# Kernel tuning notes

Hardware: AMD Instinct MI355X
Metric: run time of the kernel (lower is better)

The kernel has to match this reference:

```python
import jax, jax.numpy as jnp
import numpy as np
import math

BSZ, SEQ, DM = 2, 2048, 2048
NH, NKV, HD = 16, 8, 128
INTER = 8192
THETA = 10000.0
EPS = 1e-6
SOFTCAP = 50.0


def quant_per_token(x):
    # dynamic per-token symmetric int8 quant: scale = max|x|/127
    s = jnp.max(jnp.abs(x), axis=-1, keepdims=True) / 127.0
    s = jnp.maximum(s, 1e-8)
    q = jnp.clip(jnp.round(x / s), -127.0, 127.0)
    return q, s


def quant_weight(w):
    # per-output-channel symmetric int8 quant (rows are out channels)
    s = jnp.max(jnp.abs(w), axis=1, keepdims=True) / 127.0
    q = jnp.clip(jnp.round(w / s), -127.0, 127.0)
    return q, s


def w8a8_linear(qx, sx, w):
    # int8 GEMM with fused dequant: (qx @ qw^T) * s_act * s_weight
    qw, sw = quant_weight(w)
    return (qx @ qw.T) * sx * sw.T


def rmsnorm_quant(x, w):
    # RMSNormGeneral: w * x / sqrt(mean(x^2)+eps), then per-token quant
    var = jnp.mean(x * x, axis=-1, keepdims=True)
    y = x * jax.lax.rsqrt(var + EPS) * w
    return quant_per_token(y)


def rope_tables(seqlen, dim, theta):
    inv_freq = 1.0 / theta ** (jnp.arange(0, dim, 2, dtype=jnp.float32) / dim)
    pos = jnp.arange(seqlen, dtype=jnp.float32)
    fh = pos[:, None] * inv_freq[None, :]            # [S, dim/2]
    freqs = jnp.concatenate([fh, fh], axis=-1)       # [S, dim]
    return jnp.cos(freqs), jnp.sin(freqs)


def apply_rope(x, cos, sin):
    # x: [B, S, H, D]; rotate-half RoPE
    d2 = x.shape[-1] // 2
    rot = jnp.concatenate([-x[..., d2:], x[..., :d2]], axis=-1)
    return x * cos[None, :, None, :] + rot * sin[None, :, None, :]


def attention(q, k, v, mask, softcap):
    # q: [B, NH, S, D]; k, v: [B, NKV, S, D]
    groups = q.shape[1] // k.shape[1]
    if groups > 1:
        k = jnp.repeat(k, groups, axis=1)
        v = jnp.repeat(v, groups, axis=1)
    scores = jnp.einsum('bhqd,bhkd->bhqk', q, k) / math.sqrt(q.shape[-1])
    if softcap:
        scores = jnp.tanh(scores / softcap) * softcap
    scores = scores + mask
    attn = jax.nn.softmax(scores, axis=-1)
    out = jnp.einsum('bhqk,bhkd->bhqd', attn, v)
    return out.transpose(0, 2, 1, 3).reshape(q.shape[0], q.shape[2], -1)


def setup_inputs() -> dict:
    key = jax.random.key(0)
    ks = jax.random.split(key, 7)
    return {
        'hidden_states': jax.random.normal(ks[0], (BSZ, SEQ, DM), jnp.float32),
        'w_in_norm': jax.random.normal(ks[1], (DM,), jnp.float32) * 0.1 + 1.0,
        'w_post_norm': jax.random.normal(ks[2], (DM,), jnp.float32) * 0.1 + 1.0,
        'wqkv': jax.random.normal(ks[3], (NH * HD + 2 * NKV * HD, DM), jnp.float32) * 0.02,
        'wo': jax.random.normal(ks[4], (DM, NH * HD), jnp.float32) * 0.02,
        'w_gate_up': jax.random.normal(ks[5], (2 * INTER, DM), jnp.float32) * 0.02,
        'w_down': jax.random.normal(ks[6], (DM, INTER), jnp.float32) * 0.02,
    }


def reference(hidden_states, w_in_norm, w_post_norm, wqkv, wo, w_gate_up, w_down):
    q_dim, kv_dim = NH * HD, NKV * HD
    T = BSZ * SEQ
    x = hidden_states.reshape(T, DM)

    # --- attention block ---
    residual = x
    qx, sx = rmsnorm_quant(x, w_in_norm)
    qkv = w8a8_linear(qx, sx, wqkv)                      # [T, q_dim+2*kv_dim]
    q, k, v = jnp.split(qkv, [q_dim, q_dim + kv_dim], axis=-1)
    q = q.reshape(BSZ, SEQ, NH, HD)
    k = k.reshape(BSZ, SEQ, NKV, HD)
    v = v.reshape(BSZ, SEQ, NKV, HD).transpose(0, 2, 1, 3)

    cos, sin = rope_tables(SEQ, HD, THETA)
    q = apply_rope(q, cos, sin).transpose(0, 2, 1, 3)    # [B, NH, S, D]
    k = apply_rope(k, cos, sin).transpose(0, 2, 1, 3)    # [B, NKV, S, D]

    causal = jnp.tril(jnp.ones((SEQ, SEQ), dtype=bool))
    mask = jnp.where(causal, 0.0, -1e9).astype(jnp.float32)[None, None]
    attn_out = attention(q, k, v, mask, SOFTCAP).reshape(T, q_dim)

    qa, sa = quant_per_token(attn_out)
    x = residual + w8a8_linear(qa, sa, wo)

    # --- MLP block ---
    residual = x
    qx, sx = rmsnorm_quant(x, w_post_norm)
    gateup = w8a8_linear(qx, sx, w_gate_up)              # [T, 2*INTER]
    gate, up = jnp.split(gateup, 2, axis=-1)
    act = jax.nn.gelu(gate, approximate=True) * up       # gelu_and_mul
    qm, sm = quant_per_token(act)
    x = residual + w8a8_linear(qm, sm, w_down)

    return x.reshape(BSZ, SEQ, DM)
```

## Files before the change

### kernel.cpp

```cpp
#include <hip/hip_runtime.h>
#include <cstdint>
#include <math.h>

#define T_TOKENS 4096
#define SEQ 2048
#define DM 2048
#define NH 16
#define NKV 8
#define HD 128
#define QDIM 2048
#define KVDIM 1024
#define QKVN 4096
#define INTER 8192
#define GUN 16384

typedef int v4i __attribute__((ext_vector_type(4)));
typedef float v4f __attribute__((ext_vector_type(4)));
typedef short s8v __attribute__((ext_vector_type(8)));
typedef short s4v __attribute__((ext_vector_type(4)));
typedef short s2v __attribute__((ext_vector_type(2)));

#define GL16(g, l)                                                                       \
  __builtin_amdgcn_global_load_lds((__attribute__((address_space(1))) const void*)(g),   \
                                   (__attribute__((address_space(3))) void*)(l), 16, 0, 0)

__device__ inline float wave_sum(float v) {
#pragma unroll
  for (int off = 32; off > 0; off >>= 1) v += __shfl_down(v, off);
  return v;
}
__device__ inline float wave_max(float v) {
#pragma unroll
  for (int off = 32; off > 0; off >>= 1) v = fmaxf(v, __shfl_down(v, off));
  return v;
}
__device__ inline float dot4(float4 a, float4 b) {
  return a.x * b.x + a.y * b.y + a.z * b.z + a.w * b.w;
}
__device__ inline int8_t quant1(float v, float s) {
  float q = rintf(v / s);
  q = fminf(fmaxf(q, -127.f), 127.f);
  return (int8_t)(int)q;
}
__device__ inline unsigned short f2bf_rne(float x) {
  unsigned u = __float_as_uint(x);
  return (unsigned short)((u + 0x7FFFu + ((u >> 16) & 1u)) >> 16);
}
__device__ inline float bf2f(unsigned short h) { return __uint_as_float(((unsigned)h) << 16); }

__global__ void rope_table_kernel(float* __restrict__ cosT, float* __restrict__ sinT) {
  int s = blockIdx.x, d = threadIdx.x;
  float inv = 1.0f / powf(10000.0f, (float)d * (1.0f / 64.0f));
  float f = (float)s * inv;
  cosT[s * 64 + d] = cosf(f);
  sinT[s * 64 + d] = sinf(f);
}

__global__ __launch_bounds__(256) void quant_w_kernel(const float* __restrict__ w,
                                                      int8_t* __restrict__ qw,
                                                      float* __restrict__ sw, int K) {
  __shared__ float red[4];
  int row = blockIdx.x, tid = threadIdx.x;
  const float* wr = w + (size_t)row * K;
  int nv = K >> 10;
  float4 v[8];
  float mx = 0.f;
#pragma unroll
  for (int i = 0; i < 8; i++) {
    if (i < nv) {
      v[i] = *(const float4*)(wr + (size_t)(tid + i * 256) * 4);
      mx = fmaxf(mx, fmaxf(fmaxf(fabsf(v[i].x), fabsf(v[i].y)),
                           fmaxf(fabsf(v[i].z), fabsf(v[i].w))));
    }
  }
  mx = wave_max(mx);
  if ((tid & 63) == 0) red[tid >> 6] = mx;
  __syncthreads();
  float m = fmaxf(fmaxf(red[0], red[1]), fmaxf(red[2], red[3]));
  float s = m * (1.0f / 127.0f);
  if (tid == 0) sw[row] = s;
  float sd = (s > 0.f) ? s : 1.f;
  int8_t* qr = qw + (size_t)row * K;
#pragma unroll
  for (int i = 0; i < 8; i++) {
    if (i < nv) {
      char4 o;
      o.x = quant1(v[i].x, sd);
      o.y = quant1(v[i].y, sd);
      o.z = quant1(v[i].z, sd);
      o.w = quant1(v[i].w, sd);
      *(char4*)(qr + (size_t)(tid + i * 256) * 4) = o;
    }
  }
}

__global__ __launch_bounds__(256) void quant_w_gu_kernel(const float* __restrict__ w,
                                                         int8_t* __restrict__ qw,
                                                         float* __restrict__ sw) {
  __shared__ float red[4];
  int row = blockIdx.x, tid = threadIdx.x;
  const int K = DM;
  int j = (row < INTER) ? row : row - INTER;
  int pr = (j >> 6) * 128 + ((j >> 4) & 3) * 32 + ((row < INTER) ? 0 : 16) + (j & 15);
  const float* wr = w + (size_t)row * K;
  float4 v[2];
  float mx = 0.f;
#pragma unroll
  for (int i = 0; i < 2; i++) {
    v[i] = *(const float4*)(wr + (size_t)(tid + i * 256) * 4);
    mx = fmaxf(mx, fmaxf(fmaxf(fabsf(v[i].x), fabsf(v[i].y)),
                         fmaxf(fabsf(v[i].z), fabsf(v[i].w))));
  }
  mx = wave_max(mx);
  if ((tid & 63) == 0) red[tid >> 6] = mx;
  __syncthreads();
  float m = fmaxf(fmaxf(red[0], red[1]), fmaxf(red[2], red[3]));
  float s = m * (1.0f / 127.0f);
  if (tid == 0) sw[pr] = s;
  float sd = (s > 0.f) ? s : 1.f;
  int8_t* qr = qw + (size_t)pr * K;
#pragma unroll
  for (int i = 0; i < 2; i++) {
    char4 o;
    o.x = quant1(v[i].x, sd);
    o.y = quant1(v[i].y, sd);
    o.z = quant1(v[i].z, sd);
    o.w = quant1(v[i].w, sd);
    *(char4*)(qr + (size_t)(tid + i * 256) * 4) = o;
  }
}

__global__ __launch_bounds__(256) void rmsnorm_quant_kernel(const float* __restrict__ x,
                                                            const float* __restrict__ w,
                                                            int8_t* __restrict__ q,
                                                            float* __restrict__ s) {
  __shared__ float red[8];
  int t = blockIdx.x, tid = threadIdx.x;
  const float* xr = x + (size_t)t * DM;
  float4 a = *(const float4*)(xr + tid * 8);
  float4 b = *(const float4*)(xr + tid * 8 + 4);
  float ss = dot4(a, a) + dot4(b, b);
  ss = wave_sum(ss);
  if ((tid & 63) == 0) red[tid >> 6] = ss;
  __syncthreads();
  float tot = red[0] + red[1] + red[2] + red[3];
  float rms = rsqrtf(tot * (1.0f / DM) + 1e-6f);
  float4 wa = *(const float4*)(w + tid * 8);
  float4 wb = *(const float4*)(w + tid * 8 + 4);
  float y[8] = {a.x * rms * wa.x, a.y * rms * wa.y, a.z * rms * wa.z, a.w * rms * wa.w,
                b.x * rms * wb.x, b.y * rms * wb.y, b.z * rms * wb.z, b.w * rms * wb.w};
  float mx = 0.f;
#pragma unroll
  for (int i = 0; i < 8; i++) mx = fmaxf(mx, fabsf(y[i]));
  mx = wave_max(mx);
  if ((tid & 63) == 0) red[4 + (tid >> 6)] = mx;
  __syncthreads();
  float m = fmaxf(fmaxf(red[4], red[5]), fmaxf(red[6], red[7]));
  float sc = fmaxf(m * (1.0f / 127.0f), 1e-8f);
  if (tid == 0) s[t] = sc;
  int8_t* qr = q + (size_t)t * DM + tid * 8;
  char4 o0, o1;
  o0.x = quant1(y[0], sc); o0.y = quant1(y[1], sc); o0.z = quant1(y[2], sc); o0.w = quant1(y[3], sc);
  o1.x = quant1(y[4], sc); o1.y = quant1(y[5], sc); o1.z = quant1(y[6], sc); o1.w = quant1(y[7], sc);
  *(char4*)(qr) = o0;
  *(char4*)(qr + 4) = o1;
}

__global__ __launch_bounds__(256) void quant_rows_2048_kernel(const float* __restrict__ x,
                                                              int8_t* __restrict__ q,
                                                              float* __restrict__ s) {
  __shared__ float red[4];
  int t = blockIdx.x, tid = threadIdx.x;
  const float* xr = x + (size_t)t * DM;
  float4 a = *(const float4*)(xr + tid * 8);
  float4 b = *(const float4*)(xr + tid * 8 + 4);
  float y[8] = {a.x, a.y, a.z, a.w, b.x, b.y, b.z, b.w};
  float mx = 0.f;
#pragma unroll
  for (int i = 0; i < 8; i++) mx = fmaxf(mx, fabsf(y[i]));
  mx = wave_max(mx);
  if ((tid & 63) == 0) red[tid >> 6] = mx;
  __syncthreads();
  float m = fmaxf(fmaxf(red[0], red[1]), fmaxf(red[2], red[3]));
  float sc = fmaxf(m * (1.0f / 127.0f), 1e-8f);
  if (tid == 0) s[t] = sc;
  int8_t* qr = q + (size_t)t * DM + tid * 8;
  char4 o0, o1;
  o0.x = quant1(y[0], sc); o0.y = quant1(y[1], sc); o0.z = quant1(y[2], sc); o0.w = quant1(y[3], sc);
  o1.x = quant1(y[4], sc); o1.y = quant1(y[5], sc); o1.z = quant1(y[6], sc); o1.w = quant1(y[7], sc);
  *(char4*)(qr) = o0;
  *(char4*)(qr + 4) = o1;
}

__global__ __launch_bounds__(256) void quant_rows_8192_kernel(const float* __restrict__ x,
                                                              int8_t* __restrict__ q,
                                                              float* __restrict__ s) {
  __shared__ float red[4];
  int t = blockIdx.x, tid = threadIdx.x;
  const float* xr = x + (size_t)t * INTER + tid * 32;
  float y[32];
  float mx = 0.f;
#pragma unroll
  for (int i4 = 0; i4 < 32; i4 += 4) {
    float4 v = *(const float4*)(xr + i4);
    y[i4] = v.x; y[i4 + 1] = v.y; y[i4 + 2] = v.z; y[i4 + 3] = v.w;
    mx = fmaxf(mx, fmaxf(fmaxf(fabsf(v.x), fabsf(v.y)), fmaxf(fabsf(v.z), fabsf(v.w))));
  }
  mx = wave_max(mx);
  if ((tid & 63) == 0) red[tid >> 6] = mx;
  __syncthreads();
  float m = fmaxf(fmaxf(red[0], red[1]), fmaxf(red[2], red[3]));
  float sc = fmaxf(m * (1.0f / 127.0f), 1e-8f);
  if (tid == 0) s[t] = sc;
  int8_t* qr = q + (size_t)t * INTER + tid * 32;
#pragma unroll
  for (int i4 = 0; i4 < 32; i4 += 4) {
    char4 o;
    o.x = quant1(y[i4], sc);
    o.y = quant1(y[i4 + 1], sc);
    o.z = quant1(y[i4 + 2], sc);
    o.w = quant1(y[i4 + 3], sc);
    *(char4*)(qr + i4) = o;
  }
}

__global__ __launch_bounds__(256) void cvt_q_kernel(const float* __restrict__ qf,
                                                    const float* __restrict__ cosT,
                                                    const float* __restrict__ sinT,
                                                    unsigned short* __restrict__ Qhi,
                                                    unsigned short* __restrict__ Qlo) {
  int t = blockIdx.x, tid = threadIdx.x;
  int sp = t & (SEQ - 1);
  int h = tid >> 4, pb = (tid & 15) * 4;
  const float* row = qf + (size_t)t * QDIM + h * HD;
  float4 x0 = *(const float4*)(row + pb);
  float4 x1 = *(const float4*)(row + pb + 64);
  float4 c = *(const float4*)(cosT + sp * 64 + pb);
  float4 s = *(const float4*)(sinT + sp * 64 + pb);
  float y0[4] = {x0.x * c.x - x1.x * s.x, x0.y * c.y - x1.y * s.y, x0.z * c.z - x1.z * s.z,
                 x0.w * c.w - x1.w * s.w};
  float y1[4] = {x1.x * c.x + x0.x * s.x, x1.y * c.y + x0.y * s.y, x1.z * c.z + x0.z * s.z,
                 x1.w * c.w + x0.w * s.w};
  s4v h0, l0, h1, l1;
#pragma unroll
  for (int e = 0; e < 4; e++) {
    unsigned short hb = f2bf_rne(y0[e]);
    h0[e] = (short)hb;
    l0[e] = (short)f2bf_rne(y0[e] - bf2f(hb));
    hb = f2bf_rne(y1[e]);
    h1[e] = (short)hb;
    l1[e] = (short)f2bf_rne(y1[e] - bf2f(hb));
  }
  size_t o = (size_t)t * QDIM + h * HD + pb;
  *(s4v*)&Qhi[o] = h0;
  *(s4v*)&Qlo[o] = l0;
  *(s4v*)&Qhi[o + 64] = h1;
  *(s4v*)&Qlo[o + 64] = l1;
}

__global__ __launch_bounds__(256) void cvt_k_kernel(const float* __restrict__ kvf,
                                                    const float* __restrict__ cosT,
                                                    const float* __restrict__ sinT,
                                                    unsigned short* __restrict__ Khi,
                                                    unsigned short* __restrict__ Klo) {
  int t = blockIdx.x, tid = threadIdx.x;
  int sp = t & (SEQ - 1);
  int b = t >> 11;
  int g = tid >> 5, pb = (tid & 31) * 2;
  const float* row = kvf + (size_t)t * DM + g * HD;
  float2 x0 = *(const float2*)(row + pb);
  float2 x1 = *(const float2*)(row + pb + 64);
  float2 c = *(const float2*)(cosT + sp * 64 + pb);
  float2 s = *(const float2*)(sinT + sp * 64 + pb);
  float y0[2] = {x0.x * c.x - x1.x * s.x, x0.y * c.y - x1.y * s.y};
  float y1[2] = {x1.x * c.x + x0.x * s.x, x1.y * c.y + x0.y * s.y};
  s2v h0, l0, h1, l1;
#pragma unroll
  for (int e = 0; e < 2; e++) {
    unsigned short hb = f2bf_rne(y0[e]);
    h0[e] = (short)hb;
    l0[e] = (short)f2bf_rne(y0[e] - bf2f(hb));
    hb = f2bf_rne(y1[e]);
    h1[e] = (short)hb;
    l1[e] = (short)f2bf_rne(y1[e] - bf2f(hb));
  }
  size_t o = ((size_t)(b * NKV + g) * SEQ + sp) * HD + pb;
  *(s2v*)&Khi[o] = h0;
  *(s2v*)&Klo[o] = l0;
  *(s2v*)&Khi[o + 64] = h1;
  *(s2v*)&Klo[o + 64] = l1;
}

__global__ __launch_bounds__(256) void cvt_v_kernel(const float* __restrict__ kvf,
                                                    unsigned short* __restrict__ Vt) {
  __shared__ float vt[32][132];
  int bg = blockIdx.y;
  int b = bg >> 3, g = bg & 7;
  int s0 = blockIdx.x * 32;
  int tid = threadIdx.x;
#pragma unroll
  for (int i = 0; i < 4; i++) {
    int pos = tid + i * 256;
    int r = pos >> 5, d4 = (pos & 31) * 4;
    *(float4*)&vt[r][d4] =
        *(const float4*)(kvf + (size_t)(b * SEQ + s0 + r) * DM + KVDIM + g * HD + d4);
  }
  __syncthreads();
  int d = tid & 127, half = tid >> 7;
  unsigned short u[16];
#pragma unroll
  for (int i = 0; i < 16; i++) u[i] = f2bf_rne(vt[half * 16 + i][d]);
  unsigned short* dst =
      Vt + (size_t)bg * HD * SEQ + (size_t)(s0 >> 5) * 4096 + (half * 2) * 1024 + d * 8;
  *(s8v*)dst = *(s8v*)&u[0];
  *(s8v*)(dst + 1024) = *(s8v*)&u[8];
}

template <int BK>
__global__ __launch_bounds__(256) void gemm_i8_kernel(const int8_t* __restrict__ A,
                                                      const float* __restrict__ sA,
                                                      const int8_t* __restrict__ B,
                                                      const float* __restrict__ sB,
                                                      const float* __restrict__ res,
                                                      float* __restrict__ C, int N, int K) {
  constexpr int NCH = BK / 16;
  constexpr int RS = 4096 / BK;
  constexpr int ISS = BK / 32;
  __shared__ __align__(16) int8_t lA[128 * BK];
  __shared__ __align__(16) int8_t lB[128 * BK];
  int tid = threadIdx.x;
  unsigned nx = gridDim.x;
  unsigned hw = blockIdx.y * nx + blockIdx.x;
  unsigned nwg = nx * gridDim.y;
  unsigned work = (hw & 7) * (nwg >> 3) + (hw >> 3);
  int row0 = (int)(work / nx) * 128;
  int col0 = (int)(work % nx) * 128;
  int lane = tid & 63, wid = tid >> 6;
  int wm = (wid >> 1) * 64, wn = (wid & 1) * 64;
  int fr = lane & 15, lq = lane >> 4;

  int rT = tid / NCH;
  int cT = tid % NCH;
  int colS = ((cT ^ (rT & (NCH - 1))) << 4);
  const int8_t* gA = A + (size_t)(row0 + rT) * K + colS;
  const int8_t* gB = B + (size_t)(col0 + rT) * K + colS;
  int8_t* lAd = &lA[tid * 16];
  int8_t* lBd = &lB[tid * 16];

  int swzk = (fr & (NCH - 1)) << 4;
  int aoff[4], boff[4];
#pragma unroll
  for (int m = 0; m < 4; m++) {
    aoff[m] = (wm + m * 16 + fr) * BK;
    boff[m] = (wn + m * 16 + fr) * BK;
  }

  v4i acc[4][4];
#pragma unroll
  for (int m = 0; m < 4; m++)
#pragma unroll
    for (int n = 0; n < 4; n++) acc[m][n] = (v4i){0, 0, 0, 0};

  for (int k0 = 0; k0 < K; k0 += BK) {
#pragma unroll
    for (int i = 0; i < ISS; i++) GL16(gA + k0 + (size_t)(RS * i) * K, lAd + i * 4096);
#pragma unroll
    for (int i = 0; i < ISS; i++) GL16(gB + k0 + (size_t)(RS * i) * K, lBd + i * 4096);
    __syncthreads();
#pragma unroll
    for (int kk = 0; kk < BK / 64; kk++) {
      int kc = (kk * 64 + lq * 16) ^ swzk;
      v4i a[4], b[4];
#pragma unroll
      for (int m = 0; m < 4; m++) a[m] = *(const v4i*)&lA[aoff[m] + kc];
#pragma unroll
      for (int n = 0; n < 4; n++) b[n] = *(const v4i*)&lB[boff[n] + kc];
#pragma unroll
      for (int m = 0; m < 4; m++)
#pragma unroll
        for (int n = 0; n < 4; n++)
          acc[m][n] = __builtin_amdgcn_mfma_i32_16x16x64_i8(a[m], b[n], acc[m][n], 0, 0, 0);
    }
    __syncthreads();
  }
  int rj = lq * 4;
  int cn = fr;
#pragma unroll
  for (int m = 0; m < 4; m++) {
#pragma unroll
    for (int j = 0; j < 4; j++) {
      int rl = row0 + wm + m * 16 + rj + j;
      float sa = sA[rl];
      size_t rowoff = (size_t)rl * N;
#pragma unroll
      for (int n = 0; n < 4; n++) {
        int cg = col0 + wn + n * 16 + cn;
        float v = (float)acc[m][n][j] * sa * sB[cg];
        if (res) v += res[rowoff + cg];
        C[rowoff + cg] = v;
      }
    }
  }
}

__global__ __launch_bounds__(256) void gemm_gu_fused_kernel(const int8_t* __restrict__ A,
                                                            const float* __restrict__ sA,
                                                            const int8_t* __restrict__ B,
                                                            const float* __restrict__ sB,
                                                            float* __restrict__ act) {
  __shared__ __align__(16) int8_t lA[16384];
  __shared__ __align__(16) int8_t lB[16384];
  const int K = DM;
  int tid = threadIdx.x;
  unsigned nx = gridDim.x;
  unsigned ny = gridDim.y;
  unsigned hw = blockIdx.y * nx + blockIdx.x;
  unsigned nwg = nx * ny;
  unsigned work = (hw & 7) * (nwg >> 3) + (hw >> 3);
  int row0 = (int)(work % ny) * 128;
  int col0 = (int)(work / ny) * 128;
  int lane = tid & 63, wid = tid >> 6;
  int wm = (wid >> 1) * 64, wn = (wid & 1) * 64;
  int fr = lane & 15, lq = lane >> 4;

  int rT = tid >> 3;
  int colS = ((tid & 7) << 4) ^ ((rT & 7) << 4);
  const int8_t* gA = A + (size_t)(row0 + rT) * K + colS;
  const int8_t* gB = B + (size_t)(col0 + rT) * K + colS;
  int8_t* lAd = &lA[tid * 16];
  int8_t* lBd = &lB[tid * 16];

  int swzk = (fr & 7) << 4;
  int aoff[4], boff[4];
#pragma unroll
  for (int m = 0; m < 4; m++) {
    aoff[m] = (wm + m * 16 + fr) * 128;
    boff[m] = (wn + m * 16 + fr) * 128;
  }

  v4i acc[4][4];
#pragma unroll
  for (int m = 0; m < 4; m++)
#pragma unroll
    for (int n = 0; n < 4; n++) acc[m][n] = (v4i){0, 0, 0, 0};

  for (int k0 = 0; k0 < K; k0 += 128) {
#pragma unroll
    for (int i = 0; i < 4; i++) GL16(gA + k0 + (size_t)(32 * i) * K, lAd + i * 4096);
#pragma unroll
    for (int i = 0; i < 4; i++) GL16(gB + k0 + (size_t)(32 * i) * K, lBd + i * 4096);
    __syncthreads();
#pragma unroll
    for (int kk = 0; kk < 2; kk++) {
      int kc = (kk * 64 + lq * 16) ^ swzk;
      v4i a[4], b[4];
#pragma unroll
      for (int m = 0; m < 4; m++) a[m] = *(const v4i*)&lA[aoff[m] + kc];
#pragma unroll
      for (int n = 0; n < 4; n++) b[n] = *(const v4i*)&lB[boff[n] + kc];
#pragma unroll
      for (int m = 0; m < 4; m++)
#pragma unroll
        for (int n = 0; n < 4; n++)
          acc[m][n] = __builtin_amdgcn_mfma_i32_16x16x64_i8(a[m], b[n], acc[m][n], 0, 0, 0);
    }
    __syncthreads();
  }
  int rj = lq * 4;
  int cn = fr;
#pragma unroll
  for (int m = 0; m < 4; m++) {
#pragma unroll
    for (int j = 0; j < 4; j++) {
      int rl = row0 + wm + m * 16 + rj + j;
      float sa = sA[rl];
      size_t rowoff = (size_t)rl * INTER;
#pragma unroll
      for (int np = 0; np < 2; np++) {
        float gv = (float)acc[m][np * 2][j] * sa * sB[col0 + wn + (np * 2) * 16 + cn];
        float uv = (float)acc[m][np * 2 + 1][j] * sa * sB[col0 + wn + (np * 2 + 1) * 16 + cn];
        float inner = 0.7978845608028654f * (gv + 0.044715f * gv * gv * gv);
        float gl = 0.5f * gv * (1.0f + tanhf(inner));
        int jg = (col0 >> 1) + (wn >> 1) + np * 16 + cn;
        act[rowoff + jg] = gl * uv;
      }
    }
  }
}

__global__ __launch_bounds__(512, 2) void attn_mfma_kernel(
    const unsigned short* __restrict__ Qhi, const unsigned short* __restrict__ Qlo,
    const unsigned short* __restrict__ Khi, const unsigned short* __restrict__ Klo,
    const unsigned short* __restrict__ Vt, float* __restrict__ out) {
  __shared__ __align__(16) int8_t lkh[3][8192], lkl[3][8192], lvt[3][8192];
  __shared__ unsigned short ps[8][16][32];
  int hwid = blockIdx.y * gridDim.x + blockIdx.x;
  int work = (hwid & 7) * 64 + (hwid >> 3);
  int qt = 31 - (work & 31);
  int bg = work >> 5;
  int b = bg >> 3, g = bg & 7;
  int tid = threadIdx.x;
  int lane = tid & 63, w = tid >> 6;
  int lr = lane & 15, lq = lane >> 4;
  int h = g * 2 + (w >> 2);
  int qbase = qt * 64 + (w & 3) * 16;

  const int8_t* kbh = (const int8_t*)(Khi + (size_t)bg * SEQ * HD);
  const int8_t* kbl = (const int8_t*)(Klo + (size_t)bg * SEQ * HD);
  const int8_t* vb = (const int8_t*)(Vt + (size_t)bg * HD * SEQ);

  int xK = tid * 16;
  int sK = xK ^ (((xK >> 8) & 7) << 4);

  s8v qh[4], ql[4];
  {
    size_t qo = (size_t)(b * SEQ + qbase + lr) * QDIM + h * HD + lq * 8;
#pragma unroll
    for (int c = 0; c < 4; ++c) {
      qh[c] = *(const s8v*)(Qhi + qo + c * 32);
      ql[c] = *(const s8v*)(Qlo + qo + c * 32);
    }
  }

  v4f oacc[8];
#pragma unroll
  for (int i = 0; i < 8; ++i) oacc[i] = (v4f){0.f, 0.f, 0.f, 0.f};
  float lsum[4] = {0.f, 0.f, 0.f, 0.f};
  const float kin2 = 0.0035355339059327374f;

  int kswz = (lr & 7) << 4;
  int kcol = lq * 16;
  int vbase = lq * 2048 + lr * 16;

  int ktiles = 2 * qt + 2;

#define STAGE(kt, buf)                                  \
  do {                                                  \
    size_t kb = (size_t)(kt) * 8192;                    \
    GL16(kbh + kb + sK, &lkh[buf][xK]);                 \
    GL16(kbl + kb + sK, &lkl[buf][xK]);                 \
    GL16(vb + kb + xK, &lvt[buf][xK]);                  \
  } while (0)

  STAGE(0, 0);
  STAGE(1, 1);
  int cur = 0;
  for (int kt = 0; kt < ktiles; ++kt) {
    if (kt + 1 < ktiles) {
      asm volatile("s_waitcnt vmcnt(3)" ::: "memory");
    } else {
      asm volatile("s_waitcnt vmcnt(0)" ::: "memory");
    }
    __builtin_amdgcn_s_barrier();
    __builtin_amdgcn_sched_barrier(0);
    int stg = cur + 2;
    if (stg >= 3) stg -= 3;
    if (kt + 2 < ktiles) STAGE(kt + 2, stg);
    int kbase = kt * 32;
    if (kbase <= qbase + 15) {
      v4f sacc[2];
      __builtin_amdgcn_s_setprio(1);
#pragma unroll
      for (int t2 = 0; t2 < 2; ++t2) {
        v4f s1 = (v4f){0.f, 0.f, 0.f, 0.f};
        v4f s2 = (v4f){0.f, 0.f, 0.f, 0.f};
        v4f s3 = (v4f){0.f, 0.f, 0.f, 0.f};
        int rowb = (t2 * 16 + lr) * 256;
#pragma unroll
        for (int c = 0; c < 4; ++c) {
          int off = rowb + ((c * 64 + kcol) ^ kswz);
          s8v kh = *(const s8v*)&lkh[cur][off];
          s8v kl = *(const s8v*)&lkl[cur][off];
          s1 = __builtin_amdgcn_mfma_f32_16x16x32_bf16(qh[c], kh, s1, 0, 0, 0);
          s2 = __builtin_amdgcn_mfma_f32_16x16x32_bf16(qh[c], kl, s2, 0, 0, 0);
          s3 = __builtin_amdgcn_mfma_f32_16x16x32_bf16(ql[c], kh, s3, 0, 0, 0);
        }
        sacc[t2] = (s1 + s2) + s3;
      }
      __builtin_amdgcn_s_setprio(0);

#pragma unroll
      for (int j = 0; j < 4; ++j) {
        int qg = qbase + lq * 4 + j;
        int k0g = kbase + lr, k1g = kbase + 16 + lr;
        float z0 = __expf(sacc[0][j] * kin2);
        float z1 = __expf(sacc[1][j] * kin2);
        float e0 = __expf(-100.f * __builtin_amdgcn_rcpf(z0 + 1.f));
        float e1 = __expf(-100.f * __builtin_amdgcn_rcpf(z1 + 1.f));
        e0 = (k0g <= qg) ? e0 : 0.f;
        e1 = (k1g <= qg) ? e1 : 0.f;
        lsum[j] += e0 + e1;
        int q = lq * 4 + j;
        ps[w][q][lr] = f2bf_rne(e0);
        ps[w][q][16 + lr] = f2bf_rne(e1);
      }

      s8v pa = *(const s8v*)&ps[w][lr][lq * 8];
      __builtin_amdgcn_s_setprio(1);
#pragma unroll
      for (int dt = 0; dt < 8; ++dt) {
        s8v vh = *(const s8v*)&lvt[cur][vbase + dt * 256];
        oacc[dt] = __builtin_amdgcn_mfma_f32_16x16x32_bf16(pa, vh, oacc[dt], 0, 0, 0);
      }
      __builtin_amdgcn_s_setprio(0);
    }
    cur = (cur == 2) ? 0 : cur + 1;
  }
#undef STAGE

#pragma unroll
  for (int st = 1; st <= 8; st <<= 1)
#pragma unroll
    for (int j = 0; j < 4; ++j) lsum[j] += __shfl_xor(lsum[j], st);

  float inv[4];
#pragma unroll
  for (int j = 0; j < 4; ++j) inv[j] = 1.f / lsum[j];
  float* ob = out + (size_t)(b * SEQ + qbase) * QDIM + h * HD;
#pragma unroll
  for (int dt = 0; dt < 8; ++dt)
#pragma unroll
    for (int j = 0; j < 4; ++j)
      ob[(size_t)(lq * 4 + j) * QDIM + dt * 16 + lr] = oacc[dt][j] * inv[j];
}

extern "C" void kernel_launch(void* const* d_in, const int* in_sizes, int n_in, void* d_out,
                              int out_size, void* d_ws, size_t ws_size, hipStream_t stream) {
  (void)in_sizes; (void)n_in; (void)out_size; (void)ws_size;
  const float* hidden = (const float*)d_in[0];
  const float* w_in_norm = (const float*)d_in[1];
  const float* w_post_norm = (const float*)d_in[2];
  const float* wqkv = (const float*)d_in[3];
  const float* wo = (const float*)d_in[4];
  const float* w_gate_up = (const float*)d_in[5];
  const float* w_down = (const float*)d_in[6];
  float* out = (float*)d_out;

  char* p = (char*)d_ws;
  size_t off = 0;
  auto take = [&](size_t bytes) -> char* {
    char* r = p + off;
    off += (bytes + 255) & ~(size_t)255;
    return r;
  };
  const size_t MB = 1u << 20;
  int8_t* qx = (int8_t*)take((size_t)T_TOKENS * DM);
  float* sx = (float*)take((size_t)T_TOKENS * 4);
  int8_t* qw_qkv = (int8_t*)take((size_t)QKVN * DM);
  float* sw_qkv = (float*)take((size_t)QKVN * 4);
  int8_t* qw_wo = (int8_t*)take((size_t)DM * QDIM);
  float* sw_wo = (float*)take((size_t)DM * 4);
  int8_t* qw_gu = (int8_t*)take((size_t)GUN * DM);
  float* sw_gu = (float*)take((size_t)GUN * 4);
  int8_t* qw_dn = (int8_t*)take((size_t)DM * INTER);
  float* sw_dn = (float*)take((size_t)DM * 4);
  float* cosT = (float*)take((size_t)SEQ * 64 * 4);
  float* sinT = (float*)take((size_t)SEQ * 64 * 4);
  float* x1 = (float*)take((size_t)T_TOKENS * DM * 4);
  float* s_act = (float*)take((size_t)T_TOKENS * 4);
  char* regB = take(96 * MB);
  float* qf32 = (float*)regB;
  float* kvf32 = (float*)regB;
  float* attn_out = (float*)regB;
  unsigned short* Qhi = (unsigned short*)(regB + 32 * MB);
  unsigned short* Qlo = (unsigned short*)(regB + 48 * MB);
  unsigned short* Khi = (unsigned short*)(regB + 64 * MB);
  unsigned short* Klo = (unsigned short*)(regB + 72 * MB);
  unsigned short* Vt = (unsigned short*)(regB + 80 * MB);
  float* act_f32 = (float*)regB;
  int8_t* act_q8 = (int8_t*)(regB + 64 * MB);

  rope_table_kernel<<<SEQ, 64, 0, stream>>>(cosT, sinT);
  quant_w_kernel<<<QKVN, 256, 0, stream>>>(wqkv, qw_qkv, sw_qkv, DM);
  quant_w_kernel<<<DM, 256, 0, stream>>>(wo, qw_wo, sw_wo, QDIM);
  quant_w_gu_kernel<<<GUN, 256, 0, stream>>>(w_gate_up, qw_gu, sw_gu);
  quant_w_kernel<<<DM, 256, 0, stream>>>(w_down, qw_dn, sw_dn, INTER);

  rmsnorm_quant_kernel<<<T_TOKENS, 256, 0, stream>>>(hidden, w_in_norm, qx, sx);
  gemm_i8_kernel<256><<<dim3(QDIM / 128, T_TOKENS / 128), 256, 0, stream>>>(
      qx, sx, qw_qkv, sw_qkv, nullptr, qf32, QDIM, DM);
  cvt_q_kernel<<<T_TOKENS, 256, 0, stream>>>(qf32, cosT, sinT, Qhi, Qlo);
  gemm_i8_kernel<256><<<dim3(DM / 128, T_TOKENS / 128), 256, 0, stream>>>(
      qx, sx, qw_qkv + (size_t)QDIM * DM, sw_qkv + QDIM, nullptr, kvf32, DM, DM);
  cvt_k_kernel<<<T_TOKENS, 256, 0, stream>>>(kvf32, cosT, sinT, Khi, Klo);
  cvt_v_kernel<<<dim3(SEQ / 32, 16), 256, 0, stream>>>(kvf32, Vt);
  attn_mfma_kernel<<<dim3(SEQ / 64, 16), 512, 0, stream>>>(Qhi, Qlo, Khi, Klo, Vt, attn_out);
  quant_rows_2048_kernel<<<T_TOKENS, 256, 0, stream>>>(attn_out, qx, sx);
  gemm_i8_kernel<256><<<dim3(DM / 128, T_TOKENS / 128), 256, 0, stream>>>(
      qx, sx, qw_wo, sw_wo, hidden, x1, DM, QDIM);

  rmsnorm_quant_kernel<<<T_TOKENS, 256, 0, stream>>>(x1, w_post_norm, qx, sx);
  for (int ch = 0; ch < 4; ++ch) {
    const int8_t* qxc = qx + (size_t)ch * 1024 * DM;
    const float* sxc = sx + (size_t)ch * 1024;
    gemm_gu_fused_kernel<<<dim3(GUN / 128, 1024 / 128), 256, 0, stream>>>(qxc, sxc, qw_gu, sw_gu,
                                                                          act_f32);
    quant_rows_8192_kernel<<<1024, 256, 0, stream>>>(act_f32, act_q8 + (size_t)ch * 1024 * INTER,
                                                     s_act + (size_t)ch * 1024);
  }
  gemm_i8_kernel<256><<<dim3(DM / 128, T_TOKENS / 128), 256, 0, stream>>>(
      act_q8, s_act, qw_dn, sw_dn, x1, out, DM, INTER);
}
```

Measured before the change: 714.5 us.

## Pair short and long causal query tiles per attention block to balance work

Each attention workgroup now handles two query tiles, a short one (index pi) and its mirror long one (31-pi), sharing the streamed K/V tiles. The grid is halved to 256 blocks, each with a roughly uniform amount of causal work, and every K/V tile loaded into LDS is reused by both query tiles. The cost is doubled Q and accumulator register state per thread, which may reduce occupancy under the launch bounds, and fewer blocks in flight on the GPU.

```diff
diff --git a/kernel.cpp b/kernel.cpp
--- a/kernel.cpp
+++ b/kernel.cpp
@@ -495,15 +495,17 @@
   __shared__ __align__(16) int8_t lkh[3][8192], lkl[3][8192], lvt[3][8192];
   __shared__ unsigned short ps[8][16][32];
   int hwid = blockIdx.y * gridDim.x + blockIdx.x;
-  int work = (hwid & 7) * 64 + (hwid >> 3);
-  int qt = 31 - (work & 31);
-  int bg = work >> 5;
+  int work = (hwid & 7) * 32 + (hwid >> 3);
+  int bg = work >> 4;
+  int pi = work & 15;
+  int qtS = pi, qtL = 31 - pi;
   int b = bg >> 3, g = bg & 7;
   int tid = threadIdx.x;
   int lane = tid & 63, w = tid >> 6;
   int lr = lane & 15, lq = lane >> 4;
   int h = g * 2 + (w >> 2);
-  int qbase = qt * 64 + (w & 3) * 16;
+  int qbS = qtS * 64 + (w & 3) * 16;
+  int qbL = qtL * 64 + (w & 3) * 16;
 
   const int8_t* kbh = (const int8_t*)(Khi + (size_t)bg * SEQ * HD);
   const int8_t* kbl = (const int8_t*)(Klo + (size_t)bg * SEQ * HD);
@@ -512,27 +514,34 @@
   int xK = tid * 16;
   int sK = xK ^ (((xK >> 8) & 7) << 4);
 
-  s8v qh[4], ql[4];
+  s8v qhS[4], qlS[4], qhL[4], qlL[4];
   {
-    size_t qo = (size_t)(b * SEQ + qbase + lr) * QDIM + h * HD + lq * 8;
+    size_t qoS = (size_t)(b * SEQ + qbS + lr) * QDIM + h * HD + lq * 8;
+    size_t qoL = (size_t)(b * SEQ + qbL + lr) * QDIM + h * HD + lq * 8;
 #pragma unroll
     for (int c = 0; c < 4; ++c) {
-      qh[c] = *(const s8v*)(Qhi + qo + c * 32);
-      ql[c] = *(const s8v*)(Qlo + qo + c * 32);
-    }
-  }
-
-  v4f oacc[8];
-#pragma unroll
-  for (int i = 0; i < 8; ++i) oacc[i] = (v4f){0.f, 0.f, 0.f, 0.f};
-  float lsum[4] = {0.f, 0.f, 0.f, 0.f};
+      qhS[c] = *(const s8v*)(Qhi + qoS + c * 32);
+      qlS[c] = *(const s8v*)(Qlo + qoS + c * 32);
+      qhL[c] = *(const s8v*)(Qhi + qoL + c * 32);
+      qlL[c] = *(const s8v*)(Qlo + qoL + c * 32);
+    }
+  }
+
+  v4f oaccS[8], oaccL[8];
+#pragma unroll
+  for (int i = 0; i < 8; ++i) {
+    oaccS[i] = (v4f){0.f, 0.f, 0.f, 0.f};
+    oaccL[i] = (v4f){0.f, 0.f, 0.f, 0.f};
+  }
+  float lsumS[4] = {0.f, 0.f, 0.f, 0.f};
+  float lsumL[4] = {0.f, 0.f, 0.f, 0.f};
   const float kin2 = 0.0035355339059327374f;
 
   int kswz = (lr & 7) << 4;
   int kcol = lq * 16;
   int vbase = lq * 2048 + lr * 16;
 
-  int ktiles = 2 * qt + 2;
+  int ktiles = 2 * qtL + 2;
 
 #define STAGE(kt, buf)                                  \
   do {                                                  \
@@ -540,6 +549,49 @@
     GL16(kbh + kb + sK, &lkh[buf][xK]);                 \
     GL16(kbl + kb + sK, &lkl[buf][xK]);                 \
     GL16(vb + kb + xK, &lvt[buf][xK]);                  \
+  } while (0)
+
+#define TILE_COMPUTE(qb, qh, ql, oacc, lsum)                                           \
+  do {                                                                                 \
+    v4f sacc[2];                                                                       \
+    __builtin_amdgcn_s_setprio(1);                                                     \
+    _Pragma("unroll") for (int t2 = 0; t2 < 2; ++t2) {                                 \
+      v4f s1 = (v4f){0.f, 0.f, 0.f, 0.f};                                              \
+      v4f s2 = (v4f){0.f, 0.f, 0.f, 0.f};                                              \
+      v4f s3 = (v4f){0.f, 0.f, 0.f, 0.f};                                              \
+      int rowb = (t2 * 16 + lr) * 256;                                                 \
+      _Pragma("unroll") for (int c = 0; c < 4; ++c) {                                  \
+        int off = rowb + ((c * 64 + kcol) ^ kswz);                                     \
+        s8v kh = *(const s8v*)&lkh[cur][off];                                          \
+        s8v kl = *(const s8v*)&lkl[cur][off];                                          \
+        s1 = __builtin_amdgcn_mfma_f32_16x16x32_bf16(qh[c], kh, s1, 0, 0, 0);          \
+        s2 = __builtin_amdgcn_mfma_f32_16x16x32_bf16(qh[c], kl, s2, 0, 0, 0);          \
+        s3 = __builtin_amdgcn_mfma_f32_16x16x32_bf16(ql[c], kh, s3, 0, 0, 0);          \
+      }                                                                                \
+      sacc[t2] = (s1 + s2) + s3;                                                       \
+    }                                                                                  \
+    __builtin_amdgcn_s_setprio(0);                                                     \
+    _Pragma("unroll") for (int j = 0; j < 4; ++j) {                                    \
+      int qg = (qb) + lq * 4 + j;                                                      \
+      int k0g = kbase + lr, k1g = kbase + 16 + lr;                                     \
+      float z0 = __expf(sacc[0][j] * kin2);                                            \
+      float z1 = __expf(sacc[1][j] * kin2);                                            \
+      float e0 = __expf(-100.f * __builtin_amdgcn_rcpf(z0 + 1.f));                     \
+      float e1 = __expf(-100.f * __builtin_amdgcn_rcpf(z1 + 1.f));                     \
+      e0 = (k0g <= qg) ? e0 : 0.f;                                                     \
+      e1 = (k1g <= qg) ? e1 : 0.f;                                                     \
+      lsum[j] += e0 + e1;                                                              \
+      int q = lq * 4 + j;                                                              \
+      ps[w][q][lr] = f2bf_rne(e0);                                                     \
+      ps[w][q][16 + lr] = f2bf_rne(e1);                                                \
+    }                                                                                  \
+    s8v pa = *(const s8v*)&ps[w][lr][lq * 8];                                          \
+    __builtin_amdgcn_s_setprio(1);                                                     \
+    _Pragma("unroll") for (int dt = 0; dt < 8; ++dt) {                                 \
+      s8v vh = *(const s8v*)&lvt[cur][vbase + dt * 256];                               \
+      oacc[dt] = __builtin_amdgcn_mfma_f32_16x16x32_bf16(pa, vh, oacc[dt], 0, 0, 0);   \
+    }                                                                                  \
+    __builtin_amdgcn_s_setprio(0);                                                     \
   } while (0)
 
   STAGE(0, 0);
@@ -557,71 +609,36 @@
     if (stg >= 3) stg -= 3;
     if (kt + 2 < ktiles) STAGE(kt + 2, stg);
     int kbase = kt * 32;
-    if (kbase <= qbase + 15) {
-      v4f sacc[2];
-      __builtin_amdgcn_s_setprio(1);
-#pragma unroll
-      for (int t2 = 0; t2 < 2; ++t2) {
-        v4f s1 = (v4f){0.f, 0.f, 0.f, 0.f};
-        v4f s2 = (v4f){0.f, 0.f, 0.f, 0.f};
-        v4f s3 = (v4f){0.f, 0.f, 0.f, 0.f};
-        int rowb = (t2 * 16 + lr) * 256;
-#pragma unroll
-        for (int c = 0; c < 4; ++c) {
-          int off = rowb + ((c * 64 + kcol) ^ kswz);
-          s8v kh = *(const s8v*)&lkh[cur][off];
-          s8v kl = *(const s8v*)&lkl[cur][off];
-          s1 = __builtin_amdgcn_mfma_f32_16x16x32_bf16(qh[c], kh, s1, 0, 0, 0);
-          s2 = __builtin_amdgcn_mfma_f32_16x16x32_bf16(qh[c], kl, s2, 0, 0, 0);
-          s3 = __builtin_amdgcn_mfma_f32_16x16x32_bf16(ql[c], kh, s3, 0, 0, 0);
-        }
-        sacc[t2] = (s1 + s2) + s3;
-      }
-      __builtin_amdgcn_s_setprio(0);
-
-#pragma unroll
-      for (int j = 0; j < 4; ++j) {
-        int qg = qbase + lq * 4 + j;
-        int k0g = kbase + lr, k1g = kbase + 16 + lr;
-        float z0 = __expf(sacc[0][j] * kin2);
-        float z1 = __expf(sacc[1][j] * kin2);
-        float e0 = __expf(-100.f * __builtin_amdgcn_rcpf(z0 + 1.f));
-        float e1 = __expf(-100.f * __builtin_amdgcn_rcpf(z1 + 1.f));
-        e0 = (k0g <= qg) ? e0 : 0.f;
-        e1 = (k1g <= qg) ? e1 : 0.f;
-        lsum[j] += e0 + e1;
-        int q = lq * 4 + j;
-        ps[w][q][lr] = f2bf_rne(e0);
-        ps[w][q][16 + lr] = f2bf_rne(e1);
-      }
-
-      s8v pa = *(const s8v*)&ps[w][lr][lq * 8];
-      __builtin_amdgcn_s_setprio(1);
-#pragma unroll
-      for (int dt = 0; dt < 8; ++dt) {
-        s8v vh = *(const s8v*)&lvt[cur][vbase + dt * 256];
-        oacc[dt] = __builtin_amdgcn_mfma_f32_16x16x32_bf16(pa, vh, oacc[dt], 0, 0, 0);
-      }
-      __builtin_amdgcn_s_setprio(0);
-    }
+    TILE_COMPUTE(qbL, qhL, qlL, oaccL, lsumL);
+    if (kbase <= qbS + 15) TILE_COMPUTE(qbS, qhS, qlS, oaccS, lsumS);
     cur = (cur == 2) ? 0 : cur + 1;
   }
+#undef TILE_COMPUTE
 #undef STAGE
 
 #pragma unroll
   for (int st = 1; st <= 8; st <<= 1)
 #pragma unroll
-    for (int j = 0; j < 4; ++j) lsum[j] += __shfl_xor(lsum[j], st);
-
-  float inv[4];
-#pragma unroll
-  for (int j = 0; j < 4; ++j) inv[j] = 1.f / lsum[j];
-  float* ob = out + (size_t)(b * SEQ + qbase) * QDIM + h * HD;
+    for (int j = 0; j < 4; ++j) {
+      lsumS[j] += __shfl_xor(lsumS[j], st);
+      lsumL[j] += __shfl_xor(lsumL[j], st);
+    }
+
+  float invS[4], invL[4];
+#pragma unroll
+  for (int j = 0; j < 4; ++j) {
+    invS[j] = 1.f / lsumS[j];
+    invL[j] = 1.f / lsumL[j];
+  }
+  float* obS = out + (size_t)(b * SEQ + qbS) * QDIM + h * HD;
+  float* obL = out + (size_t)(b * SEQ + qbL) * QDIM + h * HD;
 #pragma unroll
   for (int dt = 0; dt < 8; ++dt)
 #pragma unroll
-    for (int j = 0; j < 4; ++j)
-      ob[(size_t)(lq * 4 + j) * QDIM + dt * 16 + lr] = oacc[dt][j] * inv[j];
+    for (int j = 0; j < 4; ++j) {
+      obS[(size_t)(lq * 4 + j) * QDIM + dt * 16 + lr] = oaccS[dt][j] * invS[j];
+      obL[(size_t)(lq * 4 + j) * QDIM + dt * 16 + lr] = oaccL[dt][j] * invL[j];
+    }
 }
 
 extern "C" void kernel_launch(void* const* d_in, const int* in_sizes, int n_in, void* d_out,
@@ -684,7 +701,7 @@
       qx, sx, qw_qkv + (size_t)QDIM * DM, sw_qkv + QDIM, nullptr, kvf32, DM, DM);
   cvt_k_kernel<<<T_TOKENS, 256, 0, stream>>>(kvf32, cosT, sinT, Khi, Klo);
   cvt_v_kernel<<<dim3(SEQ / 32, 16), 256, 0, stream>>>(kvf32, Vt);
-  attn_mfma_kernel<<<dim3(SEQ / 64, 16), 512, 0, stream>>>(Qhi, Qlo, Khi, Klo, Vt, attn_out);
+  attn_mfma_kernel<<<dim3(16, 16), 512, 0, stream>>>(Qhi, Qlo, Khi, Klo, Vt, attn_out);
   quant_rows_2048_kernel<<<T_TOKENS, 256, 0, stream>>>(attn_out, qx, sx);
   gemm_i8_kernel<256><<<dim3(DM / 128, T_TOKENS / 128), 256, 0, stream>>>(
       qx, sx, qw_wo, sw_wo, hidden, x1, DM, QDIM);
```

Measured after the change: 690.0 us. 3.4% less time.
